# Optimization experiments

Hardware: AMD Instinct MI355X
Metric: run time of the kernel (lower is better)

Reference implementation:

```python
import jax, jax.numpy as jnp
import numpy as np

D = 1024      # hidden_dim
H = 16        # num_heads
KV = 8        # num_kv_heads
HD = D // H   # head_size = 64
M = 3584      # intermediate_dim
E = 8         # num_local_experts
TOPK = 2      # num_experts_per_tok
EPS = 1e-6
ROPE_THETA = 10000.0


def setup_inputs() -> dict:
    key = jax.random.key(0)
    ks = jax.random.split(key, 12)
    s = 0.02
    B, S = 2, 1024
    return {
        "x": jax.random.normal(ks[0], (B, S, D), jnp.float32),
        "ln1_w": jnp.ones((D,), jnp.float32),
        "ln2_w": jnp.ones((D,), jnp.float32),
        "wq": jax.random.normal(ks[1], (D, H * HD), jnp.float32) * s,
        "wk": jax.random.normal(ks[2], (D, KV * HD), jnp.float32) * s,
        "wv": jax.random.normal(ks[3], (D, KV * HD), jnp.float32) * s,
        "wo": jax.random.normal(ks[4], (H * HD, D), jnp.float32) * s,
        "router_w": jax.random.normal(ks[5], (D, E), jnp.float32) * s,
        "w_gate": jax.random.normal(ks[6], (E, D, M), jnp.float32) * s,
        "w_up": jax.random.normal(ks[7], (E, D, M), jnp.float32) * s,
        "w_down": jax.random.normal(ks[8], (E, M, D), jnp.float32) * s,
    }


def _rmsnorm(x, w, eps=EPS):
    xf = x.astype(jnp.float32)
    var = jnp.mean(xf * xf, axis=-1, keepdims=True)
    return (xf * jax.lax.rsqrt(var + eps)).astype(x.dtype) * w


def _rope(q, k):
    # q: [B,S,H,HD], k: [B,S,KV,HD]
    S = q.shape[1]
    inv_freq = 1.0 / (ROPE_THETA ** (jnp.arange(0, HD, 2, dtype=jnp.float32) / HD))
    ang = jnp.arange(S, dtype=jnp.float32)[:, None] * inv_freq[None, :]  # [S, HD/2]
    cos = jnp.concatenate([jnp.cos(ang), jnp.cos(ang)], axis=-1)[None, :, None, :]
    sin = jnp.concatenate([jnp.sin(ang), jnp.sin(ang)], axis=-1)[None, :, None, :]

    def rot_half(t):
        t1, t2 = jnp.split(t, 2, axis=-1)
        return jnp.concatenate([-t2, t1], axis=-1)

    return q * cos + rot_half(q) * sin, k * cos + rot_half(k) * sin


def reference(x, ln1_w, ln2_w, wq, wk, wv, wo, router_w, w_gate, w_up, w_down):
    B, S, _ = x.shape

    # ---- self-attention block ----
    h = _rmsnorm(x, ln1_w)
    q = (h @ wq).reshape(B, S, H, HD)
    k = (h @ wk).reshape(B, S, KV, HD)
    v = (h @ wv).reshape(B, S, KV, HD)
    q, k = _rope(q, k)
    rep = H // KV
    k = jnp.repeat(k, rep, axis=2)  # [B,S,H,HD]
    v = jnp.repeat(v, rep, axis=2)
    scores = jnp.einsum("bqhd,bkhd->bhqk", q, k) / jnp.sqrt(jnp.float32(HD))
    causal = jnp.tril(jnp.ones((S, S), bool))
    scores = jnp.where(causal[None, None], scores, jnp.finfo(scores.dtype).min)
    attn = jax.nn.softmax(scores, axis=-1)
    ao = jnp.einsum("bhqk,bkhd->bqhd", attn, v).reshape(B, S, H * HD)
    x = x + ao @ wo

    # ---- sparse MoE block (top-2 routing, SwiGLU experts) ----
    h = _rmsnorm(x, ln2_w)
    logits = h @ router_w                       # [B,S,E]
    probs = jax.nn.softmax(logits, axis=-1)
    topv, topi = jax.lax.top_k(probs, TOPK)     # [B,S,K]
    topv = topv / jnp.sum(topv, axis=-1, keepdims=True)
    # dense combine weights [B,S,E]: zero for unselected experts
    weights = jnp.sum(jax.nn.one_hot(topi, E, dtype=h.dtype) * topv[..., None], axis=-2)
    gate = jnp.einsum("bsd,edm->bsem", h, w_gate)
    up = jnp.einsum("bsd,edm->bsem", h, w_up)
    act = jax.nn.silu(gate) * up * weights[..., None]
    moe = jnp.einsum("bsem,emd->bsd", act, w_down)
    return x + moe
```

## Files before the change

kernel.cpp:

```cpp
#include <hip/hip_runtime.h>

typedef __attribute__((ext_vector_type(8))) short short8;
typedef __attribute__((ext_vector_type(4))) float f32x4;
typedef unsigned int u32;

#define DI static __device__ __forceinline__

DI unsigned short f2bf(float f) {
  unsigned u = __builtin_bit_cast(unsigned, f);
  u += 0x7fffu + ((u >> 16) & 1u);
  return (unsigned short)(u >> 16);
}
DI float bf2f(unsigned short b) {
  unsigned u = ((unsigned)b) << 16;
  return __builtin_bit_cast(float, u);
}

DI void gload16(const unsigned short* g, unsigned short* l) {
  __builtin_amdgcn_global_load_lds(
      (const __attribute__((address_space(1))) u32*)g,
      (__attribute__((address_space(3))) u32*)l, 16, 0, 0);
}

static constexpr int NT   = 2048;
static constexpr int SEQ  = 1024;
static constexpr int DIM  = 1024;
static constexpr int NH   = 16;
static constexpr int NKV  = 8;
static constexpr int HD   = 64;
static constexpr int MDIM = 3584;
static constexpr int NE   = 8;
static constexpr int QW   = 2048;
static constexpr int GUW  = 2 * MDIM;

template <int ROWMAP>
__global__ void __launch_bounds__(256) transpose_kernel(
    const float* __restrict__ in, unsigned short* __restrict__ out,
    int R, int C, size_t in_estride, size_t out_estride) {
  __shared__ unsigned short tl[64][66];
  int e = blockIdx.z;
  const float* ip = in + (size_t)e * in_estride;
  unsigned short* op = out + (size_t)e * out_estride;
  int c0 = blockIdx.x * 64, r0 = blockIdx.y * 64;
  int tid = threadIdx.x;
  {
    int lr = tid >> 4, lc = (tid & 15) * 4;
#pragma unroll
    for (int p = 0; p < 4; ++p) {
      int r = p * 16 + lr;
      float4 v = *(const float4*)(ip + (size_t)(r0 + r) * C + c0 + lc);
      tl[lc + 0][r] = f2bf(v.x);
      tl[lc + 1][r] = f2bf(v.y);
      tl[lc + 2][r] = f2bf(v.z);
      tl[lc + 3][r] = f2bf(v.w);
    }
  }
  __syncthreads();
  {
    int c = tid >> 2, rc = (tid & 3) * 16;
    unsigned short tmp[16];
#pragma unroll
    for (int j = 0; j < 8; ++j) {
      u32 w = *(const u32*)&tl[c][rc + j * 2];
      tmp[j * 2] = (unsigned short)w;
      tmp[j * 2 + 1] = (unsigned short)(w >> 16);
    }
    int cg = c0 + c;
    int orow;
    if (ROWMAP == 0) orow = cg;
    else orow = ((cg >> 4) << 5) + (cg & 15) + (ROWMAP == 2 ? 16 : 0);
    unsigned short* dst = op + (size_t)orow * R + r0 + rc;
#pragma unroll
    for (int j = 0; j < 2; ++j)
      *(uint4*)(dst + j * 8) = *(const uint4*)&tmp[j * 8];
  }
}

__global__ void __launch_bounds__(256) vtrans_kernel(const unsigned short* __restrict__ qkv,
                                                     unsigned short* __restrict__ vT) {
  __shared__ unsigned short tl[64][66];
  int s0 = blockIdx.x * 64;
  int kvh = blockIdx.y;
  int b = blockIdx.z;
  int tid = threadIdx.x;
  {
    int r = tid >> 2, cc = (tid & 3) * 16;
    const unsigned short* src =
        qkv + ((size_t)(b * SEQ + s0 + r)) * QW + (DIM + NKV * HD + kvh * HD) + cc;
    unsigned short tmp[16];
    *(uint4*)&tmp[0] = *(const uint4*)src;
    *(uint4*)&tmp[8] = *(const uint4*)(src + 8);
#pragma unroll
    for (int j = 0; j < 16; ++j) tl[cc + j][r] = tmp[j];
  }
  __syncthreads();
  {
    int h = tid >> 2, sc = (tid & 3) * 16;
    unsigned short o[16];
#pragma unroll
    for (int j = 0; j < 16; ++j) o[j] = tl[h][sc + j];
    unsigned short* dst = vT + (((size_t)(b * NKV + kvh) * HD + h) * SEQ) + s0 + sc;
    *(uint4*)dst = *(const uint4*)&o[0];
    *(uint4*)(dst + 8) = *(const uint4*)&o[8];
  }
}

__global__ void __launch_bounds__(256) rmsnorm_kernel(const float* __restrict__ x,
                                                      const float* __restrict__ w,
                                                      unsigned short* __restrict__ out) {
  int row = blockIdx.x;
  const float* xr = x + (size_t)row * DIM;
  int i = threadIdx.x * 4;
  float4 v = *(const float4*)(xr + i);
  float s = v.x * v.x + v.y * v.y + v.z * v.z + v.w * v.w;
  for (int o = 32; o; o >>= 1) s += __shfl_xor(s, o);
  __shared__ float red[4];
  if ((threadIdx.x & 63) == 0) red[threadIdx.x >> 6] = s;
  __syncthreads();
  s = red[0] + red[1] + red[2] + red[3];
  float r = rsqrtf(s * (1.0f / DIM) + 1e-6f);
  float4 wv = *(const float4*)(w + i);
  ushort4 o4;
  o4.x = f2bf(v.x * r * wv.x);
  o4.y = f2bf(v.y * r * wv.y);
  o4.z = f2bf(v.z * r * wv.z);
  o4.w = f2bf(v.w * r * wv.w);
  *(ushort4*)(out + (size_t)row * DIM + i) = o4;
}

template <int GATHER, int EPI, int NNT>
__global__ void __launch_bounds__(256) gemmT_kernel(
    const unsigned short* __restrict__ A, int lda,
    const unsigned short* __restrict__ B, int ldb, size_t b_estride,
    void* __restrict__ Cv, int ldc,
    const float* __restrict__ resid,
    int M, int K,
    const int* __restrict__ lists, const int* __restrict__ cnt,
    int ks_count, size_t ks_stride) {
  constexpr int BN = NNT * 32;
  constexpr int NBLK = BN / 64;
  int zz = blockIdx.z;
  int e = zz / ks_count, ks = zz - e * ks_count;
  int KL = K / ks_count;
  int kbase = ks * KL;

  int count = M;
  const int* lst = nullptr;
  if (GATHER != 0) {
    count = cnt[e];
    if (count <= 0) return;
    lst = lists + e * NT;
    B += b_estride * (size_t)e;
  }
  int m0 = blockIdx.y * 128;
  if (m0 >= count) return;
  int n0 = blockIdx.x * BN;

  __shared__ unsigned short sA[3][128 * 32];
  __shared__ unsigned short sB[3][BN * 32];

  int tid = threadIdx.x, w = tid >> 6, lane = tid & 63;
  int l15 = lane & 15, lhi = lane >> 4;

  int srow = w * 16 + (lane >> 2);
  int schunk = (((lane & 3) - ((lane >> 3) & 3)) & 3) * 8;
  const unsigned short *aSrc0, *aSrc1;
  const unsigned short* bSrc[NBLK];
  {
    int mr0 = m0 + srow, mr1 = m0 + 64 + srow;
    int ar0, ar1;
    if (GATHER == 0) { ar0 = mr0; ar1 = mr1; }
    else {
      int c0i = mr0 < count ? mr0 : count - 1;
      int c1i = mr1 < count ? mr1 : count - 1;
      int p0 = lst[c0i], p1 = lst[c1i];
      ar0 = (GATHER == 1) ? (p0 >> 1) : p0;
      ar1 = (GATHER == 1) ? (p1 >> 1) : p1;
    }
    aSrc0 = A + (size_t)ar0 * lda + kbase + schunk;
    aSrc1 = A + (size_t)ar1 * lda + kbase + schunk;
#pragma unroll
    for (int s = 0; s < NBLK; ++s)
      bSrc[s] = B + (size_t)(n0 + s * 64 + srow) * ldb + kbase + schunk;
  }
  unsigned ldst = (unsigned)(w * 16) * 32;

  auto stage = [&](int buf, int k0) {
    gload16(aSrc0 + k0, &sA[buf][ldst]);
    gload16(aSrc1 + k0, &sA[buf][ldst + 64 * 32]);
#pragma unroll
    for (int s = 0; s < NBLK; ++s)
      gload16(bSrc[s] + k0, &sB[buf][ldst + s * 64 * 32]);
  };

  f32x4 acc[4][NNT] = {};
  int wm = w >> 1, wn = w & 1;
  int fslot = ((lhi + (l15 >> 1)) & 3) * 8;
  int aoff[4], boff[NNT];
#pragma unroll
  for (int t = 0; t < 4; ++t) {
    int row = wm * 64 + t * 16 + l15;
    aoff[t] = row * 32 + fslot;
  }
#pragma unroll
  for (int t = 0; t < NNT; ++t) {
    int col = wn * (BN / 2) + t * 16 + l15;
    boff[t] = col * 32 + fslot;
  }

  int nsteps = KL / 32;
  stage(0, 0);
  if (nsteps > 1) stage(1, 32);

  int cur = 0, stg = 2;
  for (int t = 0; t < nsteps; ++t) {
    if (t + 1 < nsteps) {
      if constexpr (NNT == 8) asm volatile("s_waitcnt vmcnt(6)" ::: "memory");
      else                    asm volatile("s_waitcnt vmcnt(4)" ::: "memory");
    } else {
      asm volatile("s_waitcnt vmcnt(0)" ::: "memory");
    }
    __builtin_amdgcn_s_barrier();
    __builtin_amdgcn_sched_barrier(0);
    if (t + 2 < nsteps) stage(stg, (t + 2) * 32);
    const unsigned short* pa = sA[cur];
    const unsigned short* pb = sB[cur];
    short8 af[4], bfr[NNT];
#pragma unroll
    for (int q = 0; q < 4; ++q) af[q] = *(const short8*)&pa[aoff[q]];
#pragma unroll
    for (int q = 0; q < NNT; ++q) bfr[q] = *(const short8*)&pb[boff[q]];
    __builtin_amdgcn_s_setprio(1);
#pragma unroll
    for (int mi = 0; mi < 4; ++mi)
#pragma unroll
      for (int ni = 0; ni < NNT; ++ni)
        acc[mi][ni] =
            __builtin_amdgcn_mfma_f32_16x16x32_bf16(af[mi], bfr[ni], acc[mi][ni], 0, 0, 0);
    __builtin_amdgcn_s_setprio(0);
    cur = (cur == 2) ? 0 : cur + 1;
    stg = (stg == 2) ? 0 : stg + 1;
  }

#pragma unroll
  for (int mi = 0; mi < 4; ++mi) {
#pragma unroll
    for (int r = 0; r < 4; ++r) {
      int mr = m0 + wm * 64 + mi * 16 + lhi * 4 + r;
      if (GATHER != 0 && mr >= count) continue;
      size_t crow = (GATHER != 0) ? (size_t)lst[mr] : (size_t)mr;
      if (EPI == 3) {
        float wgt = resid[crow];
        int colbase = (n0 + wn * (BN / 2)) >> 1;
#pragma unroll
        for (int ni = 0; ni < NNT; ni += 2) {
          float g = acc[mi][ni][r], u = acc[mi][ni + 1][r];
          float sv = g / (1.f + __expf(-g));
          ((unsigned short*)Cv)[crow * ldc + colbase + (ni >> 1) * 16 + l15] =
              f2bf(sv * u * wgt);
        }
      } else {
#pragma unroll
        for (int ni = 0; ni < NNT; ++ni) {
          int n = n0 + wn * (BN / 2) + ni * 16 + l15;
          float val = acc[mi][ni][r];
          if (EPI == 0)
            ((unsigned short*)Cv)[crow * ldc + n] = f2bf(val);
          else if (EPI == 1)
            ((float*)Cv)[crow * ldc + n] = val + resid[crow * ldc + n];
          else
            ((float*)Cv)[(size_t)ks * ks_stride + crow * ldc + n] = val;
        }
      }
    }
  }
}

__global__ void __launch_bounds__(256) rope_kernel(unsigned short* __restrict__ qkv) {
  int g = blockIdx.x * 256 + threadIdx.x;
  int i = g & 31;
  int hh = (g >> 5) % (NH + NKV);
  int tok = g / (32 * (NH + NKV));
  if (tok >= NT) return;
  int s = tok & (SEQ - 1);
  float inv = exp2f((float)i * (-13.287712379549449f / 32.0f));
  float ang = (float)s * inv;
  float sn = sinf(ang);
  float c = cosf(ang);
  int col = (hh < NH) ? hh * HD : DIM + (hh - NH) * HD;
  unsigned short* ptr = qkv + (size_t)tok * QW + col;
  float a = bf2f(ptr[i]), b2 = bf2f(ptr[i + 32]);
  ptr[i] = f2bf(a * c - b2 * sn);
  ptr[i + 32] = f2bf(b2 * c + a * sn);
}

__global__ void __launch_bounds__(64) attn_kernel(const unsigned short* __restrict__ qkv,
                                                  const unsigned short* __restrict__ vT,
                                                  unsigned short* __restrict__ ao) {
  __shared__ unsigned short Ps[16 * 64];
  int bid = blockIdx.x;
  int qt = bid & 63;
  int h = (bid >> 6) & 15;
  int b = bid >> 10;
  int lane = threadIdx.x, l15 = lane & 15, lhi = lane >> 4;
  int q0 = qt * 16, kvh = h >> 1;
  int kcol = DIM + kvh * HD;

  const unsigned short* qp = qkv + ((size_t)(b * SEQ + q0 + l15)) * QW + h * HD + lhi * 8;
  short8 aq0 = *(const short8*)qp;
  short8 aq1 = *(const short8*)(qp + 32);

  const unsigned short* vbase = vT + ((size_t)(b * NKV + kvh) * HD) * SEQ;

  float m[4] = {-1e30f, -1e30f, -1e30f, -1e30f};
  float l[4] = {0.f, 0.f, 0.f, 0.f};
  f32x4 accO[4] = {};

  int nkb = (qt >> 2) + 1;
  for (int kb_ = 0; kb_ < nkb; ++kb_) {
    int kbase = kb_ * 64;
    f32x4 s[4];
#pragma unroll
    for (int ct = 0; ct < 4; ++ct) {
      const unsigned short* kp =
          qkv + ((size_t)(b * SEQ + kbase + ct * 16 + l15)) * QW + kcol + lhi * 8;
      short8 k0v = *(const short8*)kp;
      short8 k1v = *(const short8*)(kp + 32);
      f32x4 a = {};
      a = __builtin_amdgcn_mfma_f32_16x16x32_bf16(aq0, k0v, a, 0, 0, 0);
      a = __builtin_amdgcn_mfma_f32_16x16x32_bf16(aq1, k1v, a, 0, 0, 0);
      int kpos = kbase + ct * 16 + l15;
#pragma unroll
      for (int r = 0; r < 4; ++r) {
        float v = a[r] * 0.125f;
        if (kpos > q0 + lhi * 4 + r) v = -1e30f;
        s[ct][r] = v;
      }
    }
    float nm[4], al[4], rs[4];
#pragma unroll
    for (int r = 0; r < 4; ++r) {
      float mb = fmaxf(fmaxf(s[0][r], s[1][r]), fmaxf(s[2][r], s[3][r]));
      mb = fmaxf(mb, __shfl_xor(mb, 1));
      mb = fmaxf(mb, __shfl_xor(mb, 2));
      mb = fmaxf(mb, __shfl_xor(mb, 4));
      mb = fmaxf(mb, __shfl_xor(mb, 8));
      nm[r] = fmaxf(m[r], mb);
      al[r] = __expf(m[r] - nm[r]);
      m[r] = nm[r];
      rs[r] = 0.f;
    }
#pragma unroll
    for (int ct = 0; ct < 4; ++ct) {
#pragma unroll
      for (int r = 0; r < 4; ++r) {
        float p = __expf(s[ct][r] - nm[r]);
        rs[r] += p;
        int q = lhi * 4 + r;
        Ps[q * 64 + ((ct * 16 + l15) ^ (lhi << 4))] = f2bf(p);
      }
    }
#pragma unroll
    for (int r = 0; r < 4; ++r) {
      rs[r] += __shfl_xor(rs[r], 1);
      rs[r] += __shfl_xor(rs[r], 2);
      rs[r] += __shfl_xor(rs[r], 4);
      rs[r] += __shfl_xor(rs[r], 8);
      l[r] = l[r] * al[r] + rs[r];
    }
#pragma unroll
    for (int dt = 0; dt < 4; ++dt)
#pragma unroll
      for (int r = 0; r < 4; ++r) accO[dt][r] *= al[r];

    int pswz = (l15 >> 2) << 4;
    short8 ap0 = *(const short8*)&Ps[l15 * 64 + ((lhi * 8) ^ pswz)];
    short8 ap1 = *(const short8*)&Ps[l15 * 64 + ((32 + lhi * 8) ^ pswz)];
#pragma unroll
    for (int dt = 0; dt < 4; ++dt) {
#pragma unroll
      for (int ks = 0; ks < 2; ++ks) {
        const unsigned short* vp =
            vbase + ((size_t)(dt * 16 + l15)) * SEQ + kbase + ks * 32 + lhi * 8;
        short8 vf = *(const short8*)vp;
        accO[dt] = __builtin_amdgcn_mfma_f32_16x16x32_bf16(ks ? ap1 : ap0, vf, accO[dt], 0, 0, 0);
      }
    }
  }
  float invl[4];
#pragma unroll
  for (int r = 0; r < 4; ++r) invl[r] = 1.f / l[r];
#pragma unroll
  for (int dt = 0; dt < 4; ++dt)
#pragma unroll
    for (int r = 0; r < 4; ++r)
      ao[((size_t)(b * SEQ + q0 + lhi * 4 + r)) * DIM + h * HD + dt * 16 + l15] =
          f2bf(accO[dt][r] * invl[r]);
}

__global__ void zero_cnt_kernel(int* __restrict__ cnt) {
  if (threadIdx.x < NE) cnt[threadIdx.x] = 0;
}

__global__ void __launch_bounds__(64) router_kernel(const float* __restrict__ x2,
                                                    const float* __restrict__ ln2w,
                                                    const float* __restrict__ rw,
                                                    float* __restrict__ wts,
                                                    int* __restrict__ cnt,
                                                    int* __restrict__ lists) {
  int t = blockIdx.x, lane = threadIdx.x;
  const float* xr = x2 + (size_t)t * DIM;
  float xs[16];
  double ssq = 0.0;
#pragma unroll
  for (int j = 0; j < 16; ++j) {
    xs[j] = xr[lane + j * 64];
    ssq += (double)xs[j] * xs[j];
  }
  for (int o = 32; o; o >>= 1) ssq += __shfl_xor(ssq, o);
  double r = rsqrt(ssq * (1.0 / DIM) + 1e-6);
  double p[NE] = {};
#pragma unroll
  for (int j = 0; j < 16; ++j) {
    int i = lane + j * 64;
    double hv = (double)xs[j] * r * (double)ln2w[i];
    const float* rwp = rw + (size_t)i * NE;
#pragma unroll
    for (int e = 0; e < NE; ++e) p[e] += hv * (double)rwp[e];
  }
  for (int o = 32; o; o >>= 1) {
#pragma unroll
    for (int e = 0; e < NE; ++e) p[e] += __shfl_xor(p[e], o);
  }
  if (lane == 0) {
    int i1 = 0;
    for (int e = 1; e < NE; ++e)
      if (p[e] > p[i1]) i1 = e;
    int i2 = (i1 == 0) ? 1 : 0;
    for (int e = 0; e < NE; ++e)
      if (e != i1 && p[e] > p[i2]) i2 = e;
    double mx = fmax(p[i1], p[i2]);
    double e1 = exp(p[i1] - mx), e2 = exp(p[i2] - mx);
    double inv = 1.0 / (e1 + e2);
    wts[t * 2] = (float)(e1 * inv);
    wts[t * 2 + 1] = (float)(e2 * inv);
    int pos1 = atomicAdd(&cnt[i1], 1);
    lists[i1 * NT + pos1] = t * 2;
    int pos2 = atomicAdd(&cnt[i2], 1);
    lists[i2 * NT + pos2] = t * 2 + 1;
  }
}

__global__ void __launch_bounds__(256) combine_kernel(const float* __restrict__ x2,
                                                      const float* __restrict__ part,
                                                      float* __restrict__ out) {
  const size_t KSS = (size_t)2 * NT * DIM;
  size_t idx = ((size_t)blockIdx.x * 256 + threadIdx.x) * 4;
  size_t t = idx >> 10;
  size_t d = idx & 1023;
  float4 o = *(const float4*)(x2 + idx);
#pragma unroll
  for (int s = 0; s < 4; ++s) {
    float4 b0 = *(const float4*)(part + s * KSS + (t * 2) * DIM + d);
    float4 c0 = *(const float4*)(part + s * KSS + (t * 2 + 1) * DIM + d);
    o.x += b0.x + c0.x;
    o.y += b0.y + c0.y;
    o.z += b0.z + c0.z;
    o.w += b0.w + c0.w;
  }
  *(float4*)(out + idx) = o;
}

extern "C" void kernel_launch(void* const* d_in, const int* in_sizes, int n_in,
                              void* d_out, int out_size, void* d_ws, size_t ws_size,
                              hipStream_t stream) {
  const float* x   = (const float*)d_in[0];
  const float* ln1 = (const float*)d_in[1];
  const float* ln2 = (const float*)d_in[2];
  const float* wq  = (const float*)d_in[3];
  const float* wk  = (const float*)d_in[4];
  const float* wv  = (const float*)d_in[5];
  const float* wo  = (const float*)d_in[6];
  const float* rw  = (const float*)d_in[7];
  const float* wg  = (const float*)d_in[8];
  const float* wu  = (const float*)d_in[9];
  const float* wd  = (const float*)d_in[10];
  float* out = (float*)d_out;

  char* p = (char*)d_ws;
  auto take = [&](size_t bytes) {
    char* q = p;
    p += (bytes + 255) & ~(size_t)255;
    return q;
  };
  unsigned short* wguT = (unsigned short*)take((size_t)NE * GUW * DIM * 2);
  unsigned short* wdT  = (unsigned short*)take((size_t)NE * DIM * MDIM * 2);
  float*          x2   = (float*)take((size_t)NT * DIM * 4);
  unsigned short* h2   = (unsigned short*)take((size_t)NT * DIM * 2);
  float*          part = (float*)take((size_t)4 * 2 * NT * DIM * 4);
  unsigned short* act  = (unsigned short*)take((size_t)2 * NT * MDIM * 2);
  float*          wtsb = (float*)take((size_t)2 * NT * 4);
  int*            cntb = (int*)take(NE * 4);
  int*            listsb = (int*)take((size_t)NE * NT * 4);
  char* X = p;
  unsigned short* wqkvT = (unsigned short*)X;
  unsigned short* woT   = wqkvT + (size_t)QW * DIM;
  unsigned short* h1    = woT + (size_t)DIM * DIM;
  unsigned short* qkv   = h1 + (size_t)NT * DIM;
  unsigned short* aob   = qkv + (size_t)NT * QW;
  unsigned short* vT    = aob + (size_t)NT * DIM;

  transpose_kernel<0><<<dim3(16, 16, 1), 256, 0, stream>>>(wq, wqkvT, DIM, DIM, 0, 0);
  transpose_kernel<0><<<dim3(8, 16, 1), 256, 0, stream>>>(wk, wqkvT + (size_t)DIM * DIM, DIM, 512, 0, 0);
  transpose_kernel<0><<<dim3(8, 16, 1), 256, 0, stream>>>(wv, wqkvT + (size_t)(DIM + 512) * DIM, DIM, 512, 0, 0);
  transpose_kernel<0><<<dim3(16, 16, 1), 256, 0, stream>>>(wo, woT, DIM, DIM, 0, 0);
  transpose_kernel<1><<<dim3(56, 16, NE), 256, 0, stream>>>(
      wg, wguT, DIM, MDIM, (size_t)DIM * MDIM, (size_t)GUW * DIM);
  transpose_kernel<2><<<dim3(56, 16, NE), 256, 0, stream>>>(
      wu, wguT, DIM, MDIM, (size_t)DIM * MDIM, (size_t)GUW * DIM);
  transpose_kernel<0><<<dim3(16, 56, NE), 256, 0, stream>>>(
      wd, wdT, MDIM, DIM, (size_t)MDIM * DIM, (size_t)DIM * MDIM);

  rmsnorm_kernel<<<NT, 256, 0, stream>>>(x, ln1, h1);
  gemmT_kernel<0, 0, 4><<<dim3(QW / 128, NT / 128, 1), 256, 0, stream>>>(
      h1, DIM, wqkvT, DIM, 0, qkv, QW, nullptr, NT, DIM, nullptr, nullptr, 1, 0);
  rope_kernel<<<(NT * (NH + NKV) * 32) / 256, 256, 0, stream>>>(qkv);
  vtrans_kernel<<<dim3(SEQ / 64, NKV, 2), 256, 0, stream>>>(qkv, vT);
  attn_kernel<<<NT * NH / 16, 64, 0, stream>>>(qkv, vT, aob);
  gemmT_kernel<0, 1, 4><<<dim3(DIM / 128, NT / 128, 1), 256, 0, stream>>>(
      aob, DIM, woT, DIM, 0, x2, DIM, x, NT, DIM, nullptr, nullptr, 1, 0);

  rmsnorm_kernel<<<NT, 256, 0, stream>>>(x2, ln2, h2);
  zero_cnt_kernel<<<1, 64, 0, stream>>>(cntb);
  router_kernel<<<NT, 64, 0, stream>>>(x2, ln2, rw, wtsb, cntb, listsb);

  gemmT_kernel<1, 3, 4><<<dim3(GUW / 128, 16, NE), 256, 0, stream>>>(
      h2, DIM, wguT, DIM, (size_t)GUW * DIM, act, MDIM, wtsb, 0, DIM, listsb, cntb, 1, 0);
  gemmT_kernel<2, 2, 4><<<dim3(DIM / 128, 16, NE * 4), 256, 0, stream>>>(
      act, MDIM, wdT, MDIM, (size_t)DIM * MDIM, part, DIM, nullptr, 0, MDIM, listsb, cntb,
      4, (size_t)2 * NT * DIM);

  combine_kernel<<<(NT * DIM) / 1024, 256, 0, stream>>>(x2, part, out);
}
```

Baseline: 507.8 us.

## Load GEMM A fragments directly from global memory and shrink attention GEMM tiles

```diff
diff --git a/kernel.cpp b/kernel.cpp
--- a/kernel.cpp
+++ b/kernel.cpp
@@ -156,52 +156,43 @@
   if (m0 >= count) return;
   int n0 = blockIdx.x * BN;
 
-  __shared__ unsigned short sA[3][128 * 32];
   __shared__ unsigned short sB[3][BN * 32];
 
   int tid = threadIdx.x, w = tid >> 6, lane = tid & 63;
   int l15 = lane & 15, lhi = lane >> 4;
+  int wm = w >> 1, wn = w & 1;
 
   int srow = w * 16 + (lane >> 2);
   int schunk = (((lane & 3) - ((lane >> 3) & 3)) & 3) * 8;
-  const unsigned short *aSrc0, *aSrc1;
   const unsigned short* bSrc[NBLK];
-  {
-    int mr0 = m0 + srow, mr1 = m0 + 64 + srow;
-    int ar0, ar1;
-    if (GATHER == 0) { ar0 = mr0; ar1 = mr1; }
-    else {
-      int c0i = mr0 < count ? mr0 : count - 1;
-      int c1i = mr1 < count ? mr1 : count - 1;
-      int p0 = lst[c0i], p1 = lst[c1i];
-      ar0 = (GATHER == 1) ? (p0 >> 1) : p0;
-      ar1 = (GATHER == 1) ? (p1 >> 1) : p1;
-    }
-    aSrc0 = A + (size_t)ar0 * lda + kbase + schunk;
-    aSrc1 = A + (size_t)ar1 * lda + kbase + schunk;
-#pragma unroll
-    for (int s = 0; s < NBLK; ++s)
-      bSrc[s] = B + (size_t)(n0 + s * 64 + srow) * ldb + kbase + schunk;
-  }
+#pragma unroll
+  for (int s = 0; s < NBLK; ++s)
+    bSrc[s] = B + (size_t)(n0 + s * 64 + srow) * ldb + kbase + schunk;
   unsigned ldst = (unsigned)(w * 16) * 32;
 
   auto stage = [&](int buf, int k0) {
-    gload16(aSrc0 + k0, &sA[buf][ldst]);
-    gload16(aSrc1 + k0, &sA[buf][ldst + 64 * 32]);
 #pragma unroll
     for (int s = 0; s < NBLK; ++s)
       gload16(bSrc[s] + k0, &sB[buf][ldst + s * 64 * 32]);
   };
 
+  const unsigned short* aFrag[4];
+#pragma unroll
+  for (int mi = 0; mi < 4; ++mi) {
+    int mr = m0 + wm * 64 + mi * 16 + l15;
+    if (mr > count - 1) mr = count - 1;
+    int ar;
+    if (GATHER == 0) ar = mr;
+    else {
+      int pid = lst[mr];
+      ar = (GATHER == 1) ? (pid >> 1) : pid;
+    }
+    aFrag[mi] = A + (size_t)ar * lda + kbase + lhi * 8;
+  }
+
   f32x4 acc[4][NNT] = {};
-  int wm = w >> 1, wn = w & 1;
   int fslot = ((lhi + (l15 >> 1)) & 3) * 8;
-  int aoff[4], boff[NNT];
-#pragma unroll
-  for (int t = 0; t < 4; ++t) {
-    int row = wm * 64 + t * 16 + l15;
-    aoff[t] = row * 32 + fslot;
-  }
+  int boff[NNT];
 #pragma unroll
   for (int t = 0; t < NNT; ++t) {
     int col = wn * (BN / 2) + t * 16 + l15;
@@ -215,19 +206,20 @@
   int cur = 0, stg = 2;
   for (int t = 0; t < nsteps; ++t) {
     if (t + 1 < nsteps) {
-      if constexpr (NNT == 8) asm volatile("s_waitcnt vmcnt(6)" ::: "memory");
-      else                    asm volatile("s_waitcnt vmcnt(4)" ::: "memory");
+      if constexpr (NBLK == 1) asm volatile("s_waitcnt vmcnt(1)" ::: "memory");
+      else                     asm volatile("s_waitcnt vmcnt(2)" ::: "memory");
     } else {
       asm volatile("s_waitcnt vmcnt(0)" ::: "memory");
     }
     __builtin_amdgcn_s_barrier();
     __builtin_amdgcn_sched_barrier(0);
+    short8 af[4];
+#pragma unroll
+    for (int mi = 0; mi < 4; ++mi)
+      af[mi] = *(const short8*)(aFrag[mi] + t * 32);
     if (t + 2 < nsteps) stage(stg, (t + 2) * 32);
-    const unsigned short* pa = sA[cur];
     const unsigned short* pb = sB[cur];
-    short8 af[4], bfr[NNT];
-#pragma unroll
-    for (int q = 0; q < 4; ++q) af[q] = *(const short8*)&pa[aoff[q]];
+    short8 bfr[NNT];
 #pragma unroll
     for (int q = 0; q < NNT; ++q) bfr[q] = *(const short8*)&pb[boff[q]];
     __builtin_amdgcn_s_setprio(1);
@@ -522,12 +514,12 @@
       wd, wdT, MDIM, DIM, (size_t)MDIM * DIM, (size_t)DIM * MDIM);
 
   rmsnorm_kernel<<<NT, 256, 0, stream>>>(x, ln1, h1);
-  gemmT_kernel<0, 0, 4><<<dim3(QW / 128, NT / 128, 1), 256, 0, stream>>>(
+  gemmT_kernel<0, 0, 2><<<dim3(QW / 64, NT / 128, 1), 256, 0, stream>>>(
       h1, DIM, wqkvT, DIM, 0, qkv, QW, nullptr, NT, DIM, nullptr, nullptr, 1, 0);
   rope_kernel<<<(NT * (NH + NKV) * 32) / 256, 256, 0, stream>>>(qkv);
   vtrans_kernel<<<dim3(SEQ / 64, NKV, 2), 256, 0, stream>>>(qkv, vT);
   attn_kernel<<<NT * NH / 16, 64, 0, stream>>>(qkv, vT, aob);
-  gemmT_kernel<0, 1, 4><<<dim3(DIM / 128, NT / 128, 1), 256, 0, stream>>>(
+  gemmT_kernel<0, 1, 2><<<dim3(DIM / 64, NT / 128, 1), 256, 0, stream>>>(
       aob, DIM, woT, DIM, 0, x2, DIM, x, NT, DIM, nullptr, nullptr, 1, 0);
 
   rmsnorm_kernel<<<NT, 256, 0, stream>>>(x2, ln2, h2);
```

Measured after the change: 617.3 us. 1.22x slower.
